# Optimization experiments

Measured on AMD Instinct MI355X. Metric: run time of the kernel, lower is better.

Reference implementation:

```python
import jax, jax.numpy as jnp
import numpy as np

HIDDEN = 4096
NUM_HEADS = 32
HEAD_DIM = HIDDEN // NUM_HEADS  # 128
ROPE_THETA = 10000.0
B, S = 1, 2048


def setup_inputs() -> dict:
    key = jax.random.key(0)
    k1, k2, k3, k4 = jax.random.split(key, 4)
    positions = jnp.broadcast_to(jnp.arange(S, dtype=jnp.int32), (B, S))
    hidden_states = jax.random.normal(k1, (B, S, HIDDEN), dtype=jnp.float32)
    # fused QKV projection (bias=True), output projection (bias=False)
    w_qkv = jax.random.normal(k2, (HIDDEN, 3 * HIDDEN), dtype=jnp.float32) * (HIDDEN ** -0.5)
    b_qkv = jax.random.normal(k3, (3 * HIDDEN,), dtype=jnp.float32) * 0.01
    w_o = jax.random.normal(k4, (HIDDEN, HIDDEN), dtype=jnp.float32) * (HIDDEN ** -0.5)
    return {"positions": positions, "hidden_states": hidden_states,
            "w_qkv": w_qkv, "b_qkv": b_qkv, "w_o": w_o}


def _apply_rope(x, positions):
    # x: [B, S, N, D]; NeoX-style rotate-half RoPE, rotary_dim == head_dim
    half = HEAD_DIM // 2
    inv_freq = 1.0 / (ROPE_THETA ** (jnp.arange(0, half, dtype=jnp.float32) / half))
    angles = positions.astype(jnp.float32)[..., None] * inv_freq  # [B, S, half]
    cos = jnp.cos(angles)[:, :, None, :]  # [B, S, 1, half]
    sin = jnp.sin(angles)[:, :, None, :]
    x1, x2 = x[..., :half], x[..., half:]
    return jnp.concatenate([x1 * cos - x2 * sin, x2 * cos + x1 * sin], axis=-1)


def reference(positions, hidden_states, w_qkv, b_qkv, w_o):
    qkv = jnp.einsum('bsh,hd->bsd', hidden_states, w_qkv) + b_qkv  # [B, S, 3H]
    q, k, v = jnp.split(qkv, 3, axis=-1)
    q = q.reshape(B, S, NUM_HEADS, HEAD_DIM)
    k = k.reshape(B, S, NUM_HEADS, HEAD_DIM)
    v = v.reshape(B, S, NUM_HEADS, HEAD_DIM)
    q = _apply_rope(q, positions)
    k = _apply_rope(k, positions)
    scale = HEAD_DIM ** -0.5
    scores = jnp.einsum('bqnd,bknd->bnqk', q, k) * scale  # [B, N, S, S]
    causal = jnp.tril(jnp.ones((S, S), dtype=bool))
    scores = jnp.where(causal, scores, jnp.finfo(scores.dtype).min)
    probs = jax.nn.softmax(scores, axis=-1)
    attn = jnp.einsum('bnqk,bknd->bqnd', probs, v).reshape(B, S, HIDDEN)
    return jnp.einsum('bsh,ho->bso', attn, w_o)
```

## Files before the change

### kernel.cpp

```cpp
#include <hip/hip_runtime.h>
#include <hip/hip_bf16.h>

#define S_LEN 2048
#define HID   4096
#define NH    32
#define HD    128
#define KD    4096

typedef __attribute__((ext_vector_type(4))) float f32x4;
typedef __attribute__((ext_vector_type(8))) short s16x8;
typedef __attribute__((ext_vector_type(4))) short s16x4;

#define AS1 __attribute__((address_space(1)))
#define AS3 __attribute__((address_space(3)))

__device__ __forceinline__ void gl_lds16(const void* g, void* l) {
  __builtin_amdgcn_global_load_lds((const AS1 void*)g, (AS3 void*)l, 16, 0, 0);
}

__device__ inline short f2bf(float f) {
  union { float f; unsigned u; } v; v.f = f;
  return (short)((v.u + 0x7fffu + ((v.u >> 16) & 1u)) >> 16);
}
__device__ inline float bf2f(short s) {
  union { unsigned u; float f; } v; v.u = ((unsigned)(unsigned short)s) << 16;
  return v.f;
}
__device__ inline unsigned packbf(float a, float b) {
  return (unsigned)(unsigned short)f2bf(a) | ((unsigned)(unsigned short)f2bf(b) << 16);
}

__global__ __launch_bounds__(256)
void cvt_kernel(const float* __restrict__ A, short* __restrict__ Ab) {
  const size_t i = ((size_t)blockIdx.x * 256 + threadIdx.x) * 8;
  f32x4 v0 = *(const f32x4*)&A[i];
  f32x4 v1 = *(const f32x4*)&A[i + 4];
  s16x8 r;
  r[0]=f2bf(v0[0]); r[1]=f2bf(v0[1]); r[2]=f2bf(v0[2]); r[3]=f2bf(v0[3]);
  r[4]=f2bf(v1[0]); r[5]=f2bf(v1[1]); r[6]=f2bf(v1[2]); r[7]=f2bf(v1[3]);
  *(s16x8*)&Ab[i] = r;
}

__global__ __launch_bounds__(256)
void transcvt_kernel(const float* __restrict__ W, short* __restrict__ Wt, const int N) {
  __shared__ float tile[64][65];
  const int k0 = blockIdx.x * 64, n0 = blockIdx.y * 64;
  const int t = threadIdx.x;
#pragma unroll
  for (int i = 0; i < 16; ++i) {
    const int e = i * 256 + t;
    const int k = e >> 6, n = e & 63;
    tile[n][k] = W[(size_t)(k0 + k) * N + n0 + n];
  }
  __syncthreads();
  const int nn = t >> 2, ks = (t & 3) * 16;
  s16x8 a, b;
#pragma unroll
  for (int i = 0; i < 8; i++) a[i] = f2bf(tile[nn][ks + i]);
#pragma unroll
  for (int i = 0; i < 8; i++) b[i] = f2bf(tile[nn][ks + 8 + i]);
  *(s16x8*)&Wt[(size_t)(n0 + nn) * KD + k0 + ks]     = a;
  *(s16x8*)&Wt[(size_t)(n0 + nn) * KD + k0 + ks + 8] = b;
}

template<int EPI>
__global__ __launch_bounds__(256, 2)
void gemm8_kernel(const short* __restrict__ A, const short* __restrict__ Bt,
                  const float* __restrict__ bias,
                  short* __restrict__ Qb, short* __restrict__ Kb, short* __restrict__ Vb,
                  float* __restrict__ Cout)
{
  __shared__ char sm[3][24576] __attribute__((aligned(128)));
  const int KD2 = KD * 2;
  const int bid = blockIdx.x;
  const int xcd = bid & 7, idx = bid >> 3;
  const int m0 = (idx & 7) * 256;
  const int n0 = (xcd * ((EPI == 0) ? 12 : 4) + (idx >> 3)) * 128;

  const int t = threadIdx.x, lane = t & 63, c = lane & 15, g = lane >> 4;
  const int w = t >> 6, wr = w >> 1, wc = w & 1;
  const int flip = ((c >> 1) & 7) << 4;
  const int laneA = wr * 8192 + ((c * 64 + g * 16) ^ flip);
  const int laneB = 16384 + wc * 4096 + ((c * 64 + g * 16) ^ flip);

  const char* srcA[4];
  const char* srcB[2];
#pragma unroll
  for (int j = 0; j < 4; ++j) {
    const int la = j * 4096 + t * 16;
    const int ls = la ^ ((la >> 3) & 0x70);
    srcA[j] = (const char*)A + (size_t)(m0 + (ls >> 6)) * KD2 + (ls & 63);
  }
#pragma unroll
  for (int j = 0; j < 2; ++j) {
    const int la = j * 4096 + t * 16;
    const int ls = la ^ ((la >> 3) & 0x70);
    srcB[j] = (const char*)Bt + (size_t)(n0 + (ls >> 6)) * KD2 + (ls & 63);
  }

  f32x4 acc[8][4];
#pragma unroll
  for (int i = 0; i < 8; i++)
#pragma unroll
    for (int j = 0; j < 4; j++) acc[i][j] = (f32x4){0.f, 0.f, 0.f, 0.f};

#define STG_H1(S, H) do {                                     \
    const size_t ko_ = (size_t)(H) * 64;                      \
    gl_lds16(srcA[0] + ko_, sm[S] + t * 16);                  \
    gl_lds16(srcA[1] + ko_, sm[S] + 4096  + t * 16);          \
    gl_lds16(srcA[2] + ko_, sm[S] + 8192  + t * 16);          \
  } while (0)
#define STG_H2(S, H) do {                                     \
    const size_t ko_ = (size_t)(H) * 64;                      \
    gl_lds16(srcA[3] + ko_, sm[S] + 12288 + t * 16);          \
    gl_lds16(srcB[0] + ko_, sm[S] + 16384 + t * 16);          \
    gl_lds16(srcB[1] + ko_, sm[S] + 20480 + t * 16);          \
  } while (0)

#define TILE8(S, S2, H, DOSTG, WN) do {                                    \
    asm volatile("s_waitcnt vmcnt(" #WN ")" ::: "memory");                 \
    __builtin_amdgcn_s_barrier();                                          \
    if (DOSTG) STG_H1(S2, H);                                              \
    const char* b_ = sm[S];                                                \
    s16x8 al_[4], bb_[4];                                                  \
    _Pragma("unroll")                                                      \
    for (int mi = 0; mi < 4; ++mi) al_[mi] = *(const s16x8*)(b_ + laneA + mi * 1024); \
    _Pragma("unroll")                                                      \
    for (int ni = 0; ni < 4; ++ni) bb_[ni] = *(const s16x8*)(b_ + laneB + ni * 1024); \
    __builtin_amdgcn_s_barrier();                                          \
    __builtin_amdgcn_s_setprio(1);                                         \
    _Pragma("unroll")                                                      \
    for (int mi = 0; mi < 4; ++mi)                                         \
      _Pragma("unroll")                                                    \
      for (int ni = 0; ni < 4; ++ni)                                       \
        acc[mi][ni] = __builtin_amdgcn_mfma_f32_16x16x32_bf16(al_[mi], bb_[ni], acc[mi][ni], 0, 0, 0); \
    __builtin_amdgcn_s_setprio(0);                                         \
    __builtin_amdgcn_s_barrier();                                          \
    if (DOSTG) STG_H2(S2, H);                                              \
    s16x8 ah_[4];                                                          \
    _Pragma("unroll")                                                      \
    for (int mi = 0; mi < 4; ++mi) ah_[mi] = *(const s16x8*)(b_ + laneA + (4 + mi) * 1024); \
    __builtin_amdgcn_s_barrier();                                          \
    __builtin_amdgcn_s_setprio(1);                                         \
    _Pragma("unroll")                                                      \
    for (int mi = 0; mi < 4; ++mi)                                         \
      _Pragma("unroll")                                                    \
      for (int ni = 0; ni < 4; ++ni)                                       \
        acc[4 + mi][ni] = __builtin_amdgcn_mfma_f32_16x16x32_bf16(ah_[mi], bb_[ni], acc[4 + mi][ni], 0, 0, 0); \
    __builtin_amdgcn_s_setprio(0);                                         \
  } while (0)

  STG_H1(0, 0); STG_H2(0, 0);
  STG_H1(1, 1); STG_H2(1, 1);
  for (int j = 0; j < 42; ++j) {
    const int h = 3 * j;
    TILE8(0, 2, h + 2, true, 6);
    TILE8(1, 0, h + 3, true, 6);
    TILE8(2, 1, h + 4, true, 6);
  }
  TILE8(0, 0, 0, false, 6);
  TILE8(1, 0, 0, false, 0);

#undef STG_H1
#undef STG_H2
#undef TILE8

  if (EPI == 0) {
#pragma unroll
    for (int ni = 0; ni < 4; ++ni) {
      const int ncol = n0 + wc * 64 + ni * 16 + c;
      const int which = ncol >> 12;
      const int h = (ncol >> 7) & 31;
      const int dcl = ncol & 127;
      short* dst = (which == 0) ? Qb : ((which == 1) ? Kb : Vb);
      const float bv = bias[ncol];
#pragma unroll
      for (int mi = 0; mi < 8; ++mi)
#pragma unroll
        for (int jj = 0; jj < 4; ++jj) {
          const int row = m0 + wr * 128 + mi * 16 + g * 4 + jj;
          dst[((size_t)h * S_LEN + row) * HD + dcl] = f2bf(acc[mi][ni][jj] + bv);
        }
    }
  } else {
#pragma unroll
    for (int ni = 0; ni < 4; ++ni) {
      const int ncol = n0 + wc * 64 + ni * 16 + c;
#pragma unroll
      for (int mi = 0; mi < 8; ++mi)
#pragma unroll
        for (int jj = 0; jj < 4; ++jj) {
          const int row = m0 + wr * 128 + mi * 16 + g * 4 + jj;
          Cout[(size_t)row * HID + ncol] = acc[mi][ni][jj];
        }
    }
  }
}

template<int EPI, int ABF16>
__global__ __launch_bounds__(256)
void gemm_kernel(const void* __restrict__ Av, const float* __restrict__ B,
                 const float* __restrict__ bias, const int N,
                 short* __restrict__ Qb, short* __restrict__ Kb, short* __restrict__ Vb,
                 float* __restrict__ Cout)
{
  __shared__ short As[128][40];
  __shared__ short Bs[128][40];
  const int m0 = blockIdx.x * 128;
  const int nb = blockIdx.y * 128;
  const int t  = threadIdx.x;
  const int w = t >> 6, lane = t & 63, c = lane & 15, g = lane >> 4;
  const int wm = (w >> 1) * 64, wn = (w & 1) * 64;

  f32x4 acc[4][4];
#pragma unroll
  for (int i = 0; i < 4; i++)
#pragma unroll
    for (int j = 0; j < 4; j++) acc[i][j] = (f32x4){0.f, 0.f, 0.f, 0.f};

  const int ar = t >> 3;
  const int ac = (t & 7) * 4;
  const int bn = t & 127;
  const int bkq = (t >> 7) * 16;

  for (int k0 = 0; k0 < KD; k0 += 32) {
#pragma unroll
    for (int rr = 0; rr < 4; rr++) {
      const int row = rr * 32 + ar;
      if (ABF16) {
        *(s16x4*)&As[row][ac] =
          *(const s16x4*)((const short*)Av + (size_t)(m0 + row) * KD + k0 + ac);
      } else {
        f32x4 v = *(const f32x4*)((const float*)Av + (size_t)(m0 + row) * KD + k0 + ac);
        s16x4 pk;
        pk[0] = f2bf(v[0]); pk[1] = f2bf(v[1]); pk[2] = f2bf(v[2]); pk[3] = f2bf(v[3]);
        *(s16x4*)&As[row][ac] = pk;
      }
    }
    const float* pB = B + (size_t)(k0 + bkq) * N + nb + bn;
    s16x8 b0, b1;
#pragma unroll
    for (int i = 0; i < 8; i++) b0[i] = f2bf(pB[(size_t)i * N]);
#pragma unroll
    for (int i = 0; i < 8; i++) b1[i] = f2bf(pB[(size_t)(i + 8) * N]);
    *(s16x8*)&Bs[bn][bkq]     = b0;
    *(s16x8*)&Bs[bn][bkq + 8] = b1;
    __syncthreads();
    s16x8 af[4], bfr[4];
#pragma unroll
    for (int i = 0; i < 4; i++) af[i]  = *(const s16x8*)&As[wm + i * 16 + c][g * 8];
#pragma unroll
    for (int i = 0; i < 4; i++) bfr[i] = *(const s16x8*)&Bs[wn + i * 16 + c][g * 8];
#pragma unroll
    for (int mi = 0; mi < 4; mi++)
#pragma unroll
      for (int ni = 0; ni < 4; ni++)
        acc[mi][ni] = __builtin_amdgcn_mfma_f32_16x16x32_bf16(af[mi], bfr[ni], acc[mi][ni], 0, 0, 0);
    __syncthreads();
  }

  if (EPI == 0) {
    const int which = nb >> 12;
    const int h = (nb & 4095) >> 7;
    short* dst = (which == 0) ? Qb : ((which == 1) ? Kb : Vb);
#pragma unroll
    for (int ni = 0; ni < 4; ni++) {
      const int d = wn + ni * 16 + c;
      const float bv = bias[nb + d];
#pragma unroll
      for (int mi = 0; mi < 4; mi++)
#pragma unroll
        for (int j = 0; j < 4; j++) {
          const int row = m0 + wm + mi * 16 + g * 4 + j;
          dst[((size_t)h * S_LEN + row) * HD + d] = f2bf(acc[mi][ni][j] + bv);
        }
    }
  } else {
#pragma unroll
    for (int ni = 0; ni < 4; ni++) {
      const int n = nb + wn + ni * 16 + c;
#pragma unroll
      for (int mi = 0; mi < 4; mi++)
#pragma unroll
        for (int j = 0; j < 4; j++) {
          const int row = m0 + wm + mi * 16 + g * 4 + j;
          Cout[(size_t)row * N + n] = acc[mi][ni][j];
        }
    }
  }
}

__global__ void rope_kernel(const int* __restrict__ positions,
                            short* __restrict__ Qb, short* __restrict__ Kb)
{
  const int s = blockIdx.x;
  const int h = blockIdx.y * 4 + threadIdx.y;
  const int d = threadIdx.x;
  const float pos = (float)positions[s];
  const float inv_freq = exp2f(-(float)d * 0.20762050593046014f);
  const float ang = pos * inv_freq;
  float sn, cs;
  sincosf(ang, &sn, &cs);
  const size_t base = ((size_t)h * S_LEN + s) * HD + d;
  const float scale = 0.08838834764831845f;
  float x1 = bf2f(Qb[base]), x2 = bf2f(Qb[base + 64]);
  Qb[base]      = f2bf((x1 * cs - x2 * sn) * scale);
  Qb[base + 64] = f2bf((x2 * cs + x1 * sn) * scale);
  x1 = bf2f(Kb[base]); x2 = bf2f(Kb[base + 64]);
  Kb[base]      = f2bf(x1 * cs - x2 * sn);
  Kb[base + 64] = f2bf(x2 * cs + x1 * sn);
}

__global__ __launch_bounds__(256)
void vtrans_kernel(const short* __restrict__ V, short* __restrict__ Vt)
{
  __shared__ short tile[64][72];
  const int h = blockIdx.z;
  const int s0 = blockIdx.x * 64;
  const int d0 = blockIdx.y * 64;
  const int tx = threadIdx.x & 63, ty = threadIdx.x >> 6;
  for (int r = ty; r < 64; r += 4)
    tile[r][tx] = V[((size_t)h * S_LEN + s0 + r) * HD + d0 + tx];
  __syncthreads();
  for (int r = ty; r < 64; r += 4)
    Vt[((size_t)h * HD + d0 + r) * S_LEN + s0 + tx] = tile[tx][r];
}

__global__ __launch_bounds__(512)
void attn_kernel(const short* __restrict__ Q, const short* __restrict__ Kg,
                 const short* __restrict__ Vtg, short* __restrict__ attn_out)
{
  __shared__ short Ks[2][64][128];
  __shared__ short Vs[2][128][72];
  const int h = blockIdx.y;
  const int ib = blockIdx.x;
  const int q0a = ib * 128;
  const int q0b = (15 - ib) * 128;
  const int nt0 = 2 * ib + 2;
  const int nt1 = 32 - 2 * ib;
  const int t = threadIdx.x;
  const int w = t >> 6, lane = t & 63, c = lane & 15, g = lane >> 4;
  const short* Qh = Q   + (size_t)h * S_LEN * HD;
  const short* Kh = Kg  + (size_t)h * S_LEN * HD;
  const short* Vh = Vtg + (size_t)h * HD * S_LEN;

  const int krow = t >> 4, kch = t & 15;
  const int vrow = t >> 3, vch = t & 7;
  const int ksw = (kch ^ ((krow & 3) | ((krow >> 1) & 4))) * 16;

  const int rbase = (c >> 2) * 8 + (c & 3);
  const int sb = (rbase & 3) | ((rbase >> 1) & 4);
  int koff[4];
#pragma unroll
  for (int di = 0; di < 4; ++di) koff[di] = ((di * 4 + g) ^ sb) * 16;

  const int qga = q0a + w * 16 + c;
  const int qgb = q0b + w * 16 + c;
  s16x8 qfa[4], qfb[4];
#pragma unroll
  for (int di = 0; di < 4; di++) {
    qfa[di] = *(const s16x8*)&Qh[(size_t)qga * HD + di * 32 + g * 8];
    qfb[di] = *(const s16x8*)&Qh[(size_t)qgb * HD + di * 32 + g * 8];
  }

  f32x4 oa[8], ob[8];
#pragma unroll
  for (int dt = 0; dt < 8; dt++) {
    oa[dt] = (f32x4){0.f, 0.f, 0.f, 0.f};
    ob[dt] = (f32x4){0.f, 0.f, 0.f, 0.f};
  }
  float m_a = -3.0e38f, l_a = 0.f, m_b = -3.0e38f, l_b = 0.f;

#define SM_PANEL(SA, SB, SC, SD, QG, FULL, MR, LR, OARR, PB0, PB1) do {        \
    float v_[16];                                                              \
    if (FULL) {                                                                \
      _Pragma("unroll")                                                        \
      for (int j = 0; j < 4; ++j) {                                            \
        v_[j] = SA[j]; v_[4 + j] = SB[j]; v_[8 + j] = SC[j]; v_[12 + j] = SD[j]; \
      }                                                                        \
    } else {                                                                   \
      _Pragma("unroll")                                                        \
      for (int j = 0; j < 4; ++j) {                                            \
        v_[j]      = (kb + 8 * g + j          <= (QG)) ? SA[j] : -__builtin_inff(); \
        v_[4 + j]  = (kb + 8 * g + 4 + j      <= (QG)) ? SB[j] : -__builtin_inff(); \
        v_[8 + j]  = (kb + 32 + 8 * g + j     <= (QG)) ? SC[j] : -__builtin_inff(); \
        v_[12 + j] = (kb + 32 + 8 * g + 4 + j <= (QG)) ? SD[j] : -__builtin_inff(); \
      }                                                                        \
    }                                                                          \
    float mx_ = v_[0];                                                         \
    _Pragma("unroll")                                                          \
    for (int ii = 1; ii < 16; ++ii) mx_ = fmaxf(mx_, v_[ii]);                  \
    mx_ = fmaxf(mx_, __shfl_xor(mx_, 16, 64));                                 \
    mx_ = fmaxf(mx_, __shfl_xor(mx_, 32, 64));                                 \
    const float mn_ = fmaxf(MR, mx_);                                          \
    if (!__all(mn_ - MR <= 8.0f)) {                                            \
      const float al_ = __expf(MR - mn_);                                      \
      LR *= al_;                                                               \
      _Pragma("unroll")                                                        \
      for (int dt = 0; dt < 8; ++dt)                                           \
        _Pragma("unroll")                                                      \
        for (int j = 0; j < 4; ++j) OARR[dt][j] *= al_;                        \
      MR = mn_;                                                                \
    }                                                                          \
    float p_[16], rs_ = 0.f;                                                   \
    _Pragma("unroll")                                                          \
    for (int ii = 0; ii < 16; ++ii) { p_[ii] = __expf(v_[ii] - MR); rs_ += p_[ii]; } \
    rs_ += __shfl_xor(rs_, 16, 64);                                            \
    rs_ += __shfl_xor(rs_, 32, 64);                                            \
    LR += rs_;                                                                 \
    union { s16x8 v8; unsigned u[4]; } pu0_, pu1_;                             \
    pu0_.u[0] = packbf(p_[0], p_[1]);   pu0_.u[1] = packbf(p_[2], p_[3]);      \
    pu0_.u[2] = packbf(p_[4], p_[5]);   pu0_.u[3] = packbf(p_[6], p_[7]);      \
    pu1_.u[0] = packbf(p_[8], p_[9]);   pu1_.u[1] = packbf(p_[10], p_[11]);    \
    pu1_.u[2] = packbf(p_[12], p_[13]); pu1_.u[3] = packbf(p_[14], p_[15]);    \
    PB0 = pu0_.v8; PB1 = pu1_.v8;                                              \
  } while (0)

  {
#pragma unroll
    for (int i = 0; i < 2; ++i) {
      s16x8 gK = *(const s16x8*)&Kh[(size_t)(i * 32 + krow) * HD + kch * 8];
      s16x8 gV = *(const s16x8*)&Vh[(size_t)(i * 64 + vrow) * S_LEN + vch * 8];
      *(s16x8*)((char*)&Ks[0][0][0] + (i * 32 + krow) * 256 + ksw) = gK;
      *(s16x8*)&Vs[0][i * 64 + vrow][vch * 8] = gV;
    }
  }
  __syncthreads();

  for (int kt = 0; kt < nt1; kt++) {
    const int cur = kt & 1;
    const int kb = kt * 64;
    const bool do0 = (kt < nt0);
    s16x8 gK0, gK1, gV0, gV1;
    if (kt + 1 < nt1) {
      gK0 = *(const s16x8*)&Kh[(size_t)(kb + 64 + krow) * HD + kch * 8];
      gK1 = *(const s16x8*)&Kh[(size_t)(kb + 96 + krow) * HD + kch * 8];
      gV0 = *(const s16x8*)&Vh[(size_t)vrow * S_LEN + kb + 64 + vch * 8];
      gV1 = *(const s16x8*)&Vh[(size_t)(64 + vrow) * S_LEN + kb + 64 + vch * 8];
    }
    f32x4 bA = (f32x4){0,0,0,0}, bB = (f32x4){0,0,0,0};
    f32x4 bC = (f32x4){0,0,0,0}, bD = (f32x4){0,0,0,0};
    f32x4 aA = (f32x4){0,0,0,0}, aB = (f32x4){0,0,0,0};
    f32x4 aC = (f32x4){0,0,0,0}, aD = (f32x4){0,0,0,0};
    const char* kbase = (const char*)&Ks[cur][0][0] + rbase * 256;
    __builtin_amdgcn_s_setprio(1);
    if (do0) {
#pragma unroll
      for (int di = 0; di < 4; ++di) {
        const char* p = kbase + koff[di];
        s16x8 kA = *(const s16x8*)(p);
        s16x8 kB = *(const s16x8*)(p + 1024);
        s16x8 kC = *(const s16x8*)(p + 8192);
        s16x8 kD = *(const s16x8*)(p + 9216);
        bA = __builtin_amdgcn_mfma_f32_16x16x32_bf16(kA, qfb[di], bA, 0, 0, 0);
        bB = __builtin_amdgcn_mfma_f32_16x16x32_bf16(kB, qfb[di], bB, 0, 0, 0);
        bC = __builtin_amdgcn_mfma_f32_16x16x32_bf16(kC, qfb[di], bC, 0, 0, 0);
        bD = __builtin_amdgcn_mfma_f32_16x16x32_bf16(kD, qfb[di], bD, 0, 0, 0);
        aA = __builtin_amdgcn_mfma_f32_16x16x32_bf16(kA, qfa[di], aA, 0, 0, 0);
        aB = __builtin_amdgcn_mfma_f32_16x16x32_bf16(kB, qfa[di], aB, 0, 0, 0);
        aC = __builtin_amdgcn_mfma_f32_16x16x32_bf16(kC, qfa[di], aC, 0, 0, 0);
        aD = __builtin_amdgcn_mfma_f32_16x16x32_bf16(kD, qfa[di], aD, 0, 0, 0);
      }
    } else {
#pragma unroll
      for (int di = 0; di < 4; ++di) {
        const char* p = kbase + koff[di];
        s16x8 kA = *(const s16x8*)(p);
        s16x8 kB = *(const s16x8*)(p + 1024);
        s16x8 kC = *(const s16x8*)(p + 8192);
        s16x8 kD = *(const s16x8*)(p + 9216);
        bA = __builtin_amdgcn_mfma_f32_16x16x32_bf16(kA, qfb[di], bA, 0, 0, 0);
        bB = __builtin_amdgcn_mfma_f32_16x16x32_bf16(kB, qfb[di], bB, 0, 0, 0);
        bC = __builtin_amdgcn_mfma_f32_16x16x32_bf16(kC, qfb[di], bC, 0, 0, 0);
        bD = __builtin_amdgcn_mfma_f32_16x16x32_bf16(kD, qfb[di], bD, 0, 0, 0);
      }
    }
    __builtin_amdgcn_s_setprio(0);
    s16x8 pb0, pb1, pa0, pa1;
    const bool fullb = (kb + 64 <= q0b);
    SM_PANEL(bA, bB, bC, bD, qgb, fullb, m_b, l_b, ob, pb0, pb1);
    if (do0) {
      const bool fulla = (kb + 64 <= q0a);
      SM_PANEL(aA, aB, aC, aD, qga, fulla, m_a, l_a, oa, pa0, pa1);
    }
    __builtin_amdgcn_s_setprio(1);
    if (do0) {
#pragma unroll
      for (int dt = 0; dt < 8; dt++) {
        s16x8 vf0 = *(const s16x8*)&Vs[cur][dt * 16 + c][g * 8];
        s16x8 vf1 = *(const s16x8*)&Vs[cur][dt * 16 + c][32 + g * 8];
        ob[dt] = __builtin_amdgcn_mfma_f32_16x16x32_bf16(vf0, pb0, ob[dt], 0, 0, 0);
        ob[dt] = __builtin_amdgcn_mfma_f32_16x16x32_bf16(vf1, pb1, ob[dt], 0, 0, 0);
        oa[dt] = __builtin_amdgcn_mfma_f32_16x16x32_bf16(vf0, pa0, oa[dt], 0, 0, 0);
        oa[dt] = __builtin_amdgcn_mfma_f32_16x16x32_bf16(vf1, pa1, oa[dt], 0, 0, 0);
      }
    } else {
#pragma unroll
      for (int dt = 0; dt < 8; dt++) {
        s16x8 vf0 = *(const s16x8*)&Vs[cur][dt * 16 + c][g * 8];
        s16x8 vf1 = *(const s16x8*)&Vs[cur][dt * 16 + c][32 + g * 8];
        ob[dt] = __builtin_amdgcn_mfma_f32_16x16x32_bf16(vf0, pb0, ob[dt], 0, 0, 0);
        ob[dt] = __builtin_amdgcn_mfma_f32_16x16x32_bf16(vf1, pb1, ob[dt], 0, 0, 0);
      }
    }
    __builtin_amdgcn_s_setprio(0);
    __syncthreads();
    if (kt + 1 < nt1) {
      *(s16x8*)((char*)&Ks[cur ^ 1][0][0] + krow * 256 + ksw)        = gK0;
      *(s16x8*)((char*)&Ks[cur ^ 1][0][0] + (32 + krow) * 256 + ksw) = gK1;
      *(s16x8*)&Vs[cur ^ 1][vrow][vch * 8]      = gV0;
      *(s16x8*)&Vs[cur ^ 1][64 + vrow][vch * 8] = gV1;
    }
    __syncthreads();
  }
#undef SM_PANEL

  const float inv_b = 1.0f / l_b;
  const float inv_a = 1.0f / l_a;
#pragma unroll
  for (int dt = 0; dt < 8; dt++) {
    s16x4 pkb, pka;
#pragma unroll
    for (int j = 0; j < 4; j++) {
      pkb[j] = f2bf(ob[dt][j] * inv_b);
      pka[j] = f2bf(oa[dt][j] * inv_a);
    }
    *(s16x4*)&attn_out[(size_t)qgb * HID + h * HD + dt * 16 + g * 4] = pkb;
    *(s16x4*)&attn_out[(size_t)qga * HID + h * HD + dt * 16 + g * 4] = pka;
  }
}

extern "C" void kernel_launch(void* const* d_in, const int* in_sizes, int n_in,
                              void* d_out, int out_size, void* d_ws, size_t ws_size,
                              hipStream_t stream)
{
  const int*   positions = (const int*)d_in[0];
  const float* hidden    = (const float*)d_in[1];
  const float* w_qkv     = (const float*)d_in[2];
  const float* b_qkv     = (const float*)d_in[3];
  const float* w_o       = (const float*)d_in[4];
  float* out = (float*)d_out;

  char* ws = (char*)d_ws;
  const size_t MB = (size_t)1 << 20;

  if (ws_size >= 224 * MB) {
    short* Ah    = (short*)(ws);
    short* Wqt   = (short*)(ws + 16 * MB);
    short* Wot   = (short*)(ws + 112 * MB);
    short* Qb    = (short*)(ws + 144 * MB);
    short* Kb    = (short*)(ws + 160 * MB);
    short* Vb    = (short*)(ws + 176 * MB);
    short* Vt    = (short*)(ws + 192 * MB);
    short* attnb = (short*)(ws + 208 * MB);

    cvt_kernel<<<4096, 256, 0, stream>>>(hidden, Ah);
    transcvt_kernel<<<dim3(KD / 64, 3 * HID / 64), 256, 0, stream>>>(w_qkv, Wqt, 3 * HID);
    transcvt_kernel<<<dim3(KD / 64, HID / 64), 256, 0, stream>>>(w_o, Wot, HID);
    gemm8_kernel<0><<<768, 256, 0, stream>>>(Ah, Wqt, b_qkv, Qb, Kb, Vb, nullptr);
    rope_kernel<<<dim3(S_LEN, NH / 4), dim3(64, 4), 0, stream>>>(positions, Qb, Kb);
    vtrans_kernel<<<dim3(S_LEN / 64, HD / 64, NH), 256, 0, stream>>>(Vb, Vt);
    attn_kernel<<<dim3(8, NH), 512, 0, stream>>>(Qb, Kb, Vt, attnb);
    gemm8_kernel<1><<<256, 256, 0, stream>>>(attnb, Wot, nullptr,
                                             nullptr, nullptr, nullptr, out);
  } else {
    short* Qb    = (short*)(ws);
    short* Kb    = (short*)(ws + 16 * MB);
    short* Vb    = (short*)(ws + 32 * MB);
    short* Vt    = (short*)(ws + 48 * MB);
    short* attnb = (short*)(ws + 64 * MB);

    gemm_kernel<0, 0><<<dim3(16, 96), 256, 0, stream>>>(hidden, w_qkv, b_qkv, 3 * HID,
                                                        Qb, Kb, Vb, nullptr);
    rope_kernel<<<dim3(S_LEN, NH / 4), dim3(64, 4), 0, stream>>>(positions, Qb, Kb);
    vtrans_kernel<<<dim3(S_LEN / 64, HD / 64, NH), 256, 0, stream>>>(Vb, Vt);
    attn_kernel<<<dim3(8, NH), 512, 0, stream>>>(Qb, Kb, Vt, attnb);
    gemm_kernel<1, 1><<<dim3(16, 32), 256, 0, stream>>>(attnb, w_o, nullptr, HID,
                                                        nullptr, nullptr, nullptr, out);
  }
}
```

Baseline: 467.5 us.

## Use 512-thread GEMM blocks with 4x4 per-wave tiles and simpler pipeline

The bf16 GEMM moves from 256 threads (4 waves, each computing 128x64) to 512 threads (8 waves, each computing 64x64) over the same 256x128 block tile. Accumulator registers per wave drop by half, and each thread now issues three staging loads per k-step instead of six. The split half-tile schedule with four barriers per step becomes one wait and one barrier before a single compute phase. The aim is more waves per CU to hide latency, at the cost of more LDS reads per MFMA and a simpler overlap of loads with compute.

```diff
diff --git a/kernel.cpp b/kernel.cpp
--- a/kernel.cpp
+++ b/kernel.cpp
@@ -64,8 +64,8 @@
 }
 
 template<int EPI>
-__global__ __launch_bounds__(256, 2)
-void gemm8_kernel(const short* __restrict__ A, const short* __restrict__ Bt,
+__global__ __launch_bounds__(512, 4)
+void gemm9_kernel(const short* __restrict__ A, const short* __restrict__ Bt,
                   const float* __restrict__ bias,
                   short* __restrict__ Qb, short* __restrict__ Kb, short* __restrict__ Vb,
                   float* __restrict__ Cout)
@@ -80,90 +80,71 @@
   const int t = threadIdx.x, lane = t & 63, c = lane & 15, g = lane >> 4;
   const int w = t >> 6, wr = w >> 1, wc = w & 1;
   const int flip = ((c >> 1) & 7) << 4;
-  const int laneA = wr * 8192 + ((c * 64 + g * 16) ^ flip);
+  const int laneA = wr * 4096 + ((c * 64 + g * 16) ^ flip);
   const int laneB = 16384 + wc * 4096 + ((c * 64 + g * 16) ^ flip);
 
-  const char* srcA[4];
-  const char* srcB[2];
-#pragma unroll
-  for (int j = 0; j < 4; ++j) {
-    const int la = j * 4096 + t * 16;
+  const char* srcA[2];
+  const char* srcB0;
+#pragma unroll
+  for (int j = 0; j < 2; ++j) {
+    const int la = j * 8192 + t * 16;
     const int ls = la ^ ((la >> 3) & 0x70);
     srcA[j] = (const char*)A + (size_t)(m0 + (ls >> 6)) * KD2 + (ls & 63);
   }
-#pragma unroll
-  for (int j = 0; j < 2; ++j) {
-    const int la = j * 4096 + t * 16;
+  {
+    const int la = t * 16;
     const int ls = la ^ ((la >> 3) & 0x70);
-    srcB[j] = (const char*)Bt + (size_t)(n0 + (ls >> 6)) * KD2 + (ls & 63);
-  }
-
-  f32x4 acc[8][4];
-#pragma unroll
-  for (int i = 0; i < 8; i++)
+    srcB0 = (const char*)Bt + (size_t)(n0 + (ls >> 6)) * KD2 + (ls & 63);
+  }
+
+  f32x4 acc[4][4];
+#pragma unroll
+  for (int i = 0; i < 4; i++)
 #pragma unroll
     for (int j = 0; j < 4; j++) acc[i][j] = (f32x4){0.f, 0.f, 0.f, 0.f};
 
-#define STG_H1(S, H) do {                                     \
+#define STG9(S, H) do {                                       \
     const size_t ko_ = (size_t)(H) * 64;                      \
     gl_lds16(srcA[0] + ko_, sm[S] + t * 16);                  \
-    gl_lds16(srcA[1] + ko_, sm[S] + 4096  + t * 16);          \
-    gl_lds16(srcA[2] + ko_, sm[S] + 8192  + t * 16);          \
+    gl_lds16(srcA[1] + ko_, sm[S] + 8192  + t * 16);          \
+    gl_lds16(srcB0   + ko_, sm[S] + 16384 + t * 16);          \
   } while (0)
-#define STG_H2(S, H) do {                                     \
-    const size_t ko_ = (size_t)(H) * 64;                      \
-    gl_lds16(srcA[3] + ko_, sm[S] + 12288 + t * 16);          \
-    gl_lds16(srcB[0] + ko_, sm[S] + 16384 + t * 16);          \
-    gl_lds16(srcB[1] + ko_, sm[S] + 20480 + t * 16);          \
-  } while (0)
-
-#define TILE8(S, S2, H, DOSTG, WN) do {                                    \
-    asm volatile("s_waitcnt vmcnt(" #WN ")" ::: "memory");                 \
-    __builtin_amdgcn_s_barrier();                                          \
-    if (DOSTG) STG_H1(S2, H);                                              \
+
+#define COMP9(S) do {                                                      \
     const char* b_ = sm[S];                                                \
-    s16x8 al_[4], bb_[4];                                                  \
+    s16x8 a_[4], bb_[4];                                                   \
     _Pragma("unroll")                                                      \
-    for (int mi = 0; mi < 4; ++mi) al_[mi] = *(const s16x8*)(b_ + laneA + mi * 1024); \
+    for (int mi = 0; mi < 4; ++mi) a_[mi] = *(const s16x8*)(b_ + laneA + mi * 1024); \
     _Pragma("unroll")                                                      \
     for (int ni = 0; ni < 4; ++ni) bb_[ni] = *(const s16x8*)(b_ + laneB + ni * 1024); \
-    __builtin_amdgcn_s_barrier();                                          \
     __builtin_amdgcn_s_setprio(1);                                         \
     _Pragma("unroll")                                                      \
     for (int mi = 0; mi < 4; ++mi)                                         \
       _Pragma("unroll")                                                    \
       for (int ni = 0; ni < 4; ++ni)                                       \
-        acc[mi][ni] = __builtin_amdgcn_mfma_f32_16x16x32_bf16(al_[mi], bb_[ni], acc[mi][ni], 0, 0, 0); \
-    __builtin_amdgcn_s_setprio(0);                                         \
-    __builtin_amdgcn_s_barrier();                                          \
-    if (DOSTG) STG_H2(S2, H);                                              \
-    s16x8 ah_[4];                                                          \
-    _Pragma("unroll")                                                      \
-    for (int mi = 0; mi < 4; ++mi) ah_[mi] = *(const s16x8*)(b_ + laneA + (4 + mi) * 1024); \
-    __builtin_amdgcn_s_barrier();                                          \
-    __builtin_amdgcn_s_setprio(1);                                         \
-    _Pragma("unroll")                                                      \
-    for (int mi = 0; mi < 4; ++mi)                                         \
-      _Pragma("unroll")                                                    \
-      for (int ni = 0; ni < 4; ++ni)                                       \
-        acc[4 + mi][ni] = __builtin_amdgcn_mfma_f32_16x16x32_bf16(ah_[mi], bb_[ni], acc[4 + mi][ni], 0, 0, 0); \
+        acc[mi][ni] = __builtin_amdgcn_mfma_f32_16x16x32_bf16(a_[mi], bb_[ni], acc[mi][ni], 0, 0, 0); \
     __builtin_amdgcn_s_setprio(0);                                         \
   } while (0)
 
-  STG_H1(0, 0); STG_H2(0, 0);
-  STG_H1(1, 1); STG_H2(1, 1);
+#define WAIT3 asm volatile("s_waitcnt vmcnt(3)" ::: "memory")
+#define WAIT0 asm volatile("s_waitcnt vmcnt(0)" ::: "memory")
+#define BARR  do { __builtin_amdgcn_s_barrier(); asm volatile("" ::: "memory"); } while (0)
+
+  STG9(0, 0); STG9(1, 1);
   for (int j = 0; j < 42; ++j) {
     const int h = 3 * j;
-    TILE8(0, 2, h + 2, true, 6);
-    TILE8(1, 0, h + 3, true, 6);
-    TILE8(2, 1, h + 4, true, 6);
-  }
-  TILE8(0, 0, 0, false, 6);
-  TILE8(1, 0, 0, false, 0);
-
-#undef STG_H1
-#undef STG_H2
-#undef TILE8
+    WAIT3; BARR; STG9(2, h + 2); COMP9(0);
+    WAIT3; BARR; STG9(0, h + 3); COMP9(1);
+    WAIT3; BARR; STG9(1, h + 4); COMP9(2);
+  }
+  WAIT3; BARR; COMP9(0);
+  WAIT0; BARR; COMP9(1);
+
+#undef STG9
+#undef COMP9
+#undef WAIT3
+#undef WAIT0
+#undef BARR
 
   if (EPI == 0) {
 #pragma unroll
@@ -175,10 +156,10 @@
       short* dst = (which == 0) ? Qb : ((which == 1) ? Kb : Vb);
       const float bv = bias[ncol];
 #pragma unroll
-      for (int mi = 0; mi < 8; ++mi)
+      for (int mi = 0; mi < 4; ++mi)
 #pragma unroll
         for (int jj = 0; jj < 4; ++jj) {
-          const int row = m0 + wr * 128 + mi * 16 + g * 4 + jj;
+          const int row = m0 + wr * 64 + mi * 16 + g * 4 + jj;
           dst[((size_t)h * S_LEN + row) * HD + dcl] = f2bf(acc[mi][ni][jj] + bv);
         }
     }
@@ -187,10 +168,10 @@
     for (int ni = 0; ni < 4; ++ni) {
       const int ncol = n0 + wc * 64 + ni * 16 + c;
 #pragma unroll
-      for (int mi = 0; mi < 8; ++mi)
+      for (int mi = 0; mi < 4; ++mi)
 #pragma unroll
         for (int jj = 0; jj < 4; ++jj) {
-          const int row = m0 + wr * 128 + mi * 16 + g * 4 + jj;
+          const int row = m0 + wr * 64 + mi * 16 + g * 4 + jj;
           Cout[(size_t)row * HID + ncol] = acc[mi][ni][jj];
         }
     }
@@ -557,11 +538,11 @@
     cvt_kernel<<<4096, 256, 0, stream>>>(hidden, Ah);
     transcvt_kernel<<<dim3(KD / 64, 3 * HID / 64), 256, 0, stream>>>(w_qkv, Wqt, 3 * HID);
     transcvt_kernel<<<dim3(KD / 64, HID / 64), 256, 0, stream>>>(w_o, Wot, HID);
-    gemm8_kernel<0><<<768, 256, 0, stream>>>(Ah, Wqt, b_qkv, Qb, Kb, Vb, nullptr);
+    gemm9_kernel<0><<<768, 512, 0, stream>>>(Ah, Wqt, b_qkv, Qb, Kb, Vb, nullptr);
     rope_kernel<<<dim3(S_LEN, NH / 4), dim3(64, 4), 0, stream>>>(positions, Qb, Kb);
     vtrans_kernel<<<dim3(S_LEN / 64, HD / 64, NH), 256, 0, stream>>>(Vb, Vt);
     attn_kernel<<<dim3(8, NH), 512, 0, stream>>>(Qb, Kb, Vt, attnb);
-    gemm8_kernel<1><<<256, 256, 0, stream>>>(attnb, Wot, nullptr,
+    gemm9_kernel<1><<<256, 512, 0, stream>>>(attnb, Wot, nullptr,
                                              nullptr, nullptr, nullptr, out);
   } else {
     short* Qb    = (short*)(ws);
```

Result: no change. 468.1 us (+0.1%).
